# Kernel tuning notes

Hardware: AMD Instinct MI355X
Metric: run time of the kernel (lower is better)

Reference implementation:

```python
import math
import jax, jax.numpy as jnp
import numpy as np

B, T, C = 2, 2048, 4096
H = 32
D = C // H  # head_dim = 128


def compute_freq(dim, max_len, theta=10000):
    freq = 1.0 / theta ** (jnp.arange(0, dim, 2, dtype=jnp.float32) / dim)
    t = jnp.arange(max_len, dtype=jnp.float32)
    m = jnp.einsum('i,j->ij', t, freq)          # [L, dim/2]
    m = jnp.concatenate([m, m], axis=-1)         # [L, dim]
    return jnp.cos(m), jnp.sin(m)


def rotate_half(x):
    # Faithful to source: depth = full last dim, so x1 is the whole tensor
    # and x2 is empty -> rotate_half(x) == x (a quirk of the original code).
    depth = x.shape[-1]
    x1 = x[..., :depth]
    x2 = x[..., depth:]
    return jnp.concatenate([-x2, x1], axis=-1)


def setup_inputs() -> dict:
    key = jax.random.key(0)
    kx, kq, kk, kv, ko = jax.random.split(key, 5)
    std = 0.02
    input_ids = jax.random.normal(kx, (B, T, C), dtype=jnp.float32)
    Wq = jax.random.normal(kq, (C, C), dtype=jnp.float32) * std
    Wk = jax.random.normal(kk, (C, C), dtype=jnp.float32) * std
    Wv = jax.random.normal(kv, (C, C), dtype=jnp.float32) * std
    Wo = jax.random.normal(ko, (C, C), dtype=jnp.float32) * std
    # Additive causal mask, as typically passed to this module.
    causal = jnp.tril(jnp.ones((T, T), dtype=bool))
    attention_mask = jnp.where(causal, 0.0, -1e9).astype(jnp.float32)[None, None]
    return {"input_ids": input_ids, "Wq": Wq, "Wk": Wk, "Wv": Wv,
            "Wo": Wo, "attention_mask": attention_mask}


def reference(input_ids, Wq, Wk, Wv, Wo, attention_mask):
    b, t, c = input_ids.shape
    # QKV projections (no bias), reshape to [b, h, t, d]
    q = (input_ids @ Wq).reshape(b, t, H, D).swapaxes(1, 2)
    k = (input_ids @ Wk).reshape(b, t, H, D).swapaxes(1, 2)
    v = (input_ids @ Wv).reshape(b, t, H, D).swapaxes(1, 2)
    # Inline RoPE (faithful, including the source's rotate_half behavior)
    cos, sin = compute_freq(D, t)                # [t, D]
    q = q * cos + rotate_half(q) * sin
    k = k * cos + rotate_half(k) * sin
    # Naive full attention
    attn = jnp.einsum('bhqd,bhkd->bhqk', q, k) / math.sqrt(D)
    attn = attn + attention_mask
    attn = jax.nn.softmax(attn, axis=-1)
    out = jnp.einsum('bhqk,bhkd->bhqd', attn, v)
    out = out.swapaxes(1, 2).reshape(b, t, c)
    return out @ Wo
```

## Files before the change

kernel.cpp:

```cpp
#include <hip/hip_runtime.h>
#include <hip/hip_bf16.h>

#define B_ 2
#define T_ 2048
#define C_ 4096
#define H_ 32
#define D_ 128

typedef __bf16 bf16x8 __attribute__((ext_vector_type(8)));
typedef float f32x4 __attribute__((ext_vector_type(4)));

__device__ __forceinline__ void gload_lds16(const void* g, void* l) {
  __builtin_amdgcn_global_load_lds(
      (const __attribute__((address_space(1))) void*)g,
      (__attribute__((address_space(3))) void*)l, 16, 0, 0);
}

__device__ __forceinline__ ushort f2bf(float f) {
  union { float f; uint u; } x; x.f = f;
  uint r = x.u + 0x7FFFu + ((x.u >> 16) & 1u);
  return (ushort)(r >> 16);
}

__global__ __launch_bounds__(256) void cvt_f32_bf16(
    const float* __restrict__ in, ushort* __restrict__ out)
{
  long i = ((long)blockIdx.x * 256 + threadIdx.x) * 8;
  float4 a = *(const float4*)&in[i];
  float4 b = *(const float4*)&in[i + 4];
  union { ushort u[8]; uint4 v; } g;
  g.u[0] = f2bf(a.x); g.u[1] = f2bf(a.y); g.u[2] = f2bf(a.z); g.u[3] = f2bf(a.w);
  g.u[4] = f2bf(b.x); g.u[5] = f2bf(b.y); g.u[6] = f2bf(b.z); g.u[7] = f2bf(b.w);
  *(uint4*)&out[i] = g.v;
}

__global__ __launch_bounds__(256) void transpose_f32_bf16(
    const float* __restrict__ in, ushort* __restrict__ out, int ldi, int ldo)
{
  __shared__ __align__(16) ushort tile[64][72];
  const float* ip = in + (long)blockIdx.y * 64 * ldi + (long)blockIdx.x * 64;
  ushort* op = out + (long)blockIdx.x * 64 * ldo + (long)blockIdx.y * 64;
  const int t = threadIdx.x;
  const int row = t >> 2, c0 = (t & 3) * 16;
#pragma unroll
  for (int v = 0; v < 4; ++v) {
    float4 f = *(const float4*)&ip[(long)row * ldi + c0 + v * 4];
    ushort4 w;
    w.x = f2bf(f.x); w.y = f2bf(f.y); w.z = f2bf(f.z); w.w = f2bf(f.w);
    *(ushort4*)&tile[row][c0 + v * 4] = w;
  }
  __syncthreads();
#pragma unroll
  for (int i = 0; i < 2; ++i) {
    int t2 = i * 256 + t;
    int orow = t2 >> 3, ch = t2 & 7;
    union { ushort u[8]; uint4 v; } g;
#pragma unroll
    for (int e = 0; e < 8; ++e) g.u[e] = tile[ch * 8 + e][orow];
    *(uint4*)&op[(long)orow * ldo + ch * 8] = g.v;
  }
}

__global__ __launch_bounds__(256) void transpose_bf16(
    const ushort* __restrict__ in, ushort* __restrict__ out,
    int ldi, int ldo, long zi1, long zi2, long zo1, long zo2)
{
  __shared__ __align__(16) ushort tile[64][72];
  const int z = blockIdx.z;
  const long z1 = z & 31, z2 = z >> 5;
  const ushort* ip = in + z1 * zi1 + z2 * zi2 +
                     (long)blockIdx.y * 64 * ldi + (long)blockIdx.x * 64;
  ushort* op = out + z1 * zo1 + z2 * zo2 +
               (long)blockIdx.x * 64 * ldo + (long)blockIdx.y * 64;
  const int t = threadIdx.x;
#pragma unroll
  for (int i = 0; i < 2; ++i) {
    int t2 = i * 256 + t;
    int row = t2 >> 3, ch = t2 & 7;
    *(uint4*)&tile[row][ch * 8] = *(const uint4*)&ip[(long)row * ldi + ch * 8];
  }
  __syncthreads();
#pragma unroll
  for (int i = 0; i < 2; ++i) {
    int t2 = i * 256 + t;
    int orow = t2 >> 3, ch = t2 & 7;
    union { ushort u[8]; uint4 v; } g;
#pragma unroll
    for (int e = 0; e < 8; ++e) g.u[e] = tile[ch * 8 + e][orow];
    *(uint4*)&op[(long)orow * ldo + ch * 8] = g.v;
  }
}

#define STAGE_A(h, tt) do {                                                    \
    __hip_bfloat16* dst_ = AS + ((((tt) & 1) * 2 + (h)) * 8192) + w * 512;     \
    const __hip_bfloat16* src_ = Asrc + (size_t)((h) * 128) * K + (size_t)(tt) * 64; \
    gload_lds16(src_, dst_);                                                   \
    gload_lds16(src_ + (size_t)64 * K, dst_ + 4096);                           \
  } while (0)

#define STAGE_B(h, tt) do {                                                    \
    __hip_bfloat16* dst_ = BS + ((((tt) & 1) * 2 + (h)) * 8192) + w * 512;     \
    const __hip_bfloat16* src_ = Bsrc + (size_t)((h) * 128) * K + (size_t)(tt) * 64; \
    gload_lds16(src_, dst_);                                                   \
    gload_lds16(src_ + (size_t)64 * K, dst_ + 4096);                           \
  } while (0)

#define MFMA16(pM, pN, AF, BF)                                                 \
  _Pragma("unroll")                                                            \
  for (int mf = 0; mf < 4; ++mf)                                               \
    _Pragma("unroll")                                                          \
    for (int nf = 0; nf < 2; ++nf)                                             \
      _Pragma("unroll")                                                        \
      for (int ks = 0; ks < 2; ++ks)                                           \
        acc[pM][pN][mf][nf] = __builtin_amdgcn_mfma_f32_16x16x32_bf16(         \
            AF[mf][ks], BF[nf][ks], acc[pM][pN][mf][nf], 0, 0, 0);

template <typename OutT>
__global__ __launch_bounds__(512, 2) void gemm256(
    const __hip_bfloat16* __restrict__ A,
    const __hip_bfloat16* __restrict__ Bt,
    OutT* __restrict__ C,
    int M, int N, int K, int rope_mode)
{
  extern __shared__ __hip_bfloat16 smem[];
  __hip_bfloat16* AS = smem;
  __hip_bfloat16* BS = smem + 32768;

  const int tid = threadIdx.x, lane = tid & 63, w = tid >> 6;
  const int wm = w >> 2, wn = w & 3;
  const int fr = lane & 15, quad = lane >> 4;

  const int bid = blockIdx.x;
  const int s = (bid & 7) * 32 + (bid >> 3);
  const int m0 = (s >> 4) * 256, n0 = (s & 15) * 256;

  const int srow = tid >> 3;
  const int schunk = ((tid & 7) ^ (srow & 7)) * 8;
  const __hip_bfloat16* Asrc = A + (size_t)(m0 + srow) * K + schunk;
  const __hip_bfloat16* Bsrc = Bt + (size_t)(n0 + srow) * K + schunk;

  f32x4 acc[2][2][4][2] = {};

  STAGE_A(0, 0); STAGE_B(0, 0); STAGE_A(1, 0); STAGE_B(1, 0);
  STAGE_A(0, 1); STAGE_B(0, 1); STAGE_A(1, 1); STAGE_B(1, 1);
  asm volatile("s_waitcnt vmcnt(8)" ::: "memory");
  asm volatile("s_barrier" ::: "memory");

  const int NT = K >> 6;
  for (int t = 0; t < NT; ++t) {
    const __hip_bfloat16* As0 = AS + (t & 1) * 16384;
    const __hip_bfloat16* Bs0 = BS + (t & 1) * 16384;
    bf16x8 af[4][2], b0[2][2], b1[2][2];

#pragma unroll
    for (int mf = 0; mf < 4; ++mf) {
      const int row = wm * 64 + mf * 16 + fr;
#pragma unroll
      for (int ks = 0; ks < 2; ++ks)
        af[mf][ks] = *(const bf16x8*)
            &As0[row * 64 + (((ks * 4 + quad) ^ (fr & 7)) << 3)];
    }
#pragma unroll
    for (int nf = 0; nf < 2; ++nf) {
      const int row = wn * 32 + nf * 16 + fr;
#pragma unroll
      for (int ks = 0; ks < 2; ++ks)
        b0[nf][ks] = *(const bf16x8*)
            &Bs0[row * 64 + (((ks * 4 + quad) ^ (fr & 7)) << 3)];
    }
    asm volatile("s_barrier" ::: "memory");
    asm volatile("s_waitcnt lgkmcnt(0)" ::: "memory");
    __builtin_amdgcn_sched_barrier(0);
    __builtin_amdgcn_s_setprio(1);
    MFMA16(0, 0, af, b0)
    __builtin_amdgcn_s_setprio(0);
    __builtin_amdgcn_sched_barrier(0);
    asm volatile("s_barrier" ::: "memory");

#pragma unroll
    for (int nf = 0; nf < 2; ++nf) {
      const int row = wn * 32 + nf * 16 + fr;
#pragma unroll
      for (int ks = 0; ks < 2; ++ks)
        b1[nf][ks] = *(const bf16x8*)
            &Bs0[8192 + row * 64 + (((ks * 4 + quad) ^ (fr & 7)) << 3)];
    }
    if (t + 2 < NT) { STAGE_B(0, t + 2); STAGE_A(0, t + 2); }
    asm volatile("s_barrier" ::: "memory");
    asm volatile("s_waitcnt lgkmcnt(0)" ::: "memory");
    __builtin_amdgcn_sched_barrier(0);
    __builtin_amdgcn_s_setprio(1);
    MFMA16(0, 1, af, b1)
    __builtin_amdgcn_s_setprio(0);
    __builtin_amdgcn_sched_barrier(0);
    asm volatile("s_barrier" ::: "memory");

#pragma unroll
    for (int mf = 0; mf < 4; ++mf) {
      const int row = wm * 64 + mf * 16 + fr;
#pragma unroll
      for (int ks = 0; ks < 2; ++ks)
        af[mf][ks] = *(const bf16x8*)
            &As0[8192 + row * 64 + (((ks * 4 + quad) ^ (fr & 7)) << 3)];
    }
    if (t + 2 < NT) STAGE_B(1, t + 2);
    asm volatile("s_barrier" ::: "memory");
    asm volatile("s_waitcnt lgkmcnt(0)" ::: "memory");
    __builtin_amdgcn_sched_barrier(0);
    __builtin_amdgcn_s_setprio(1);
    MFMA16(1, 1, af, b1)
    __builtin_amdgcn_s_setprio(0);
    __builtin_amdgcn_sched_barrier(0);
    asm volatile("s_barrier" ::: "memory");

    if (t + 2 < NT) STAGE_A(1, t + 2);
    if (t < NT - 2) asm volatile("s_waitcnt vmcnt(8)" ::: "memory");
    else            asm volatile("s_waitcnt vmcnt(0)" ::: "memory");
    asm volatile("s_barrier" ::: "memory");
    __builtin_amdgcn_sched_barrier(0);
    __builtin_amdgcn_s_setprio(1);
    MFMA16(1, 0, af, b0)
    __builtin_amdgcn_s_setprio(0);
    __builtin_amdgcn_sched_barrier(0);
    asm volatile("s_barrier" ::: "memory");
  }

  const float gscale = (rope_mode == 1) ? 0.08838834764831845f : 1.0f;
  float freqv[2] = {0.f, 0.f};
  if (rope_mode) {
#pragma unroll
    for (int nf = 0; nf < 2; ++nf)
      freqv[nf] = exp2f((float)((wn & 1) * 32 + nf * 16 + fr) *
                        -0.20762050593046012f);
  }
#pragma unroll
  for (int pM = 0; pM < 2; ++pM)
#pragma unroll
    for (int mf = 0; mf < 4; ++mf)
#pragma unroll
      for (int r = 0; r < 4; ++r) {
        const int grow = m0 + pM * 128 + wm * 64 + mf * 16 + quad * 4 + r;
        float fct[2] = {1.f, 1.f};
        if (rope_mode) {
          const int tt = grow & (T_ - 1);
#pragma unroll
          for (int nf = 0; nf < 2; ++nf) {
            float sn, cs;
            sincosf((float)tt * freqv[nf], &sn, &cs);
            fct[nf] = (cs + sn) * gscale;
          }
        }
#pragma unroll
        for (int pN = 0; pN < 2; ++pN)
#pragma unroll
          for (int nf = 0; nf < 2; ++nf) {
            const int col = n0 + pN * 128 + wn * 32 + nf * 16 + fr;
            float v = acc[pM][pN][mf][nf][r] * fct[nf];
            if constexpr (sizeof(OutT) == 4)
              C[(size_t)grow * N + col] = v;
            else
              C[(size_t)grow * N + col] = __float2bfloat16(v);
          }
      }
}

__global__ __launch_bounds__(256, 3) void flash_attn(
    const __hip_bfloat16* __restrict__ Q,
    const __hip_bfloat16* __restrict__ K,
    const __hip_bfloat16* __restrict__ Vt,
    __hip_bfloat16* __restrict__ O)
{
  __shared__ __align__(16) __hip_bfloat16 Ks[128 * 128];
  __shared__ __align__(16) __hip_bfloat16 Ps[4][32 * 64];
  const int tid = threadIdx.x, lane = tid & 63, wid = tid >> 6;
  const int bx = blockIdx.x, bh = blockIdx.y;
  const int b = bh >> 5, h = bh & 31;
  const int fr = lane & 15, fq = (lane >> 4) * 8;
  const int quad = lane >> 4;
  const __hip_bfloat16* Kbase = K + (size_t)(b * T_) * C_ + h * D_;
  const __hip_bfloat16* Vbase = Vt + (size_t)bh * D_ * T_;

  const int strow = wid * 32 + quad;

  for (int pass = 0; pass < 2; ++pass) {
    const int qt = pass ? (15 - bx) : bx;
    const int q0 = qt * 128;
    const __hip_bfloat16* Qbase = Q + (size_t)(b * T_ + q0) * C_ + h * D_;

#pragma unroll
    for (int j = 0; j < 8; ++j) {
      const int swz = quad + (j & 1) * 4;
      gload_lds16(Qbase + (size_t)(strow + j * 4) * C_ + ((fr ^ swz) * 8),
                  &Ks[(wid * 8 + j) * 512]);
    }
    __syncthreads();
    bf16x8 qf[2][4];
#pragma unroll
    for (int mi = 0; mi < 2; ++mi)
#pragma unroll
      for (int ks = 0; ks < 4; ++ks)
        qf[mi][ks] = *(const bf16x8*)&Ks[(wid * 32 + mi * 16 + fr) * 128 +
                                         (((ks * 4 + quad) ^ (fr & 7)) << 3)];
    __syncthreads();

    float m_i[2][4], l_i[2][4];
#pragma unroll
    for (int mi = 0; mi < 2; ++mi)
#pragma unroll
      for (int r = 0; r < 4; ++r) { m_i[mi][r] = -1e30f; l_i[mi][r] = 0.f; }
    f32x4 oa[2][8] = {};

    for (int kt = 0; kt <= qt; ++kt) {
#pragma unroll
      for (int j = 0; j < 8; ++j) {
        const int swz = quad + (j & 1) * 4;
        gload_lds16(
            Kbase + (size_t)(kt * 128 + strow + j * 4) * C_ + ((fr ^ swz) * 8),
            &Ks[(wid * 8 + j) * 512]);
      }
      __syncthreads();

      f32x4 s[2][8] = {};
#pragma unroll
      for (int ks = 0; ks < 4; ++ks) {
        bf16x8 kf[8];
#pragma unroll
        for (int ni = 0; ni < 8; ++ni)
          kf[ni] = *(const bf16x8*)&Ks[(ni * 16 + fr) * 128 +
                                       (((ks * 4 + quad) ^ (fr & 7)) << 3)];
        __builtin_amdgcn_s_setprio(1);
#pragma unroll
        for (int mi = 0; mi < 2; ++mi)
#pragma unroll
          for (int ni = 0; ni < 8; ++ni)
            s[mi][ni] = __builtin_amdgcn_mfma_f32_16x16x32_bf16(
                qf[mi][ks], kf[ni], s[mi][ni], 0, 0, 0);
        __builtin_amdgcn_s_setprio(0);
      }
      __syncthreads();

#pragma unroll
      for (int j = 0; j < 8; ++j) {
        const int swz = quad + (j & 1) * 4;
        gload_lds16(
            Vbase + (size_t)(strow + j * 4) * T_ + kt * 128 + ((fr ^ swz) * 8),
            &Ks[(wid * 8 + j) * 512]);
      }

      if (kt == qt) {
#pragma unroll
        for (int mi = 0; mi < 2; ++mi)
#pragma unroll
          for (int ni = 0; ni < 8; ++ni)
#pragma unroll
            for (int r = 0; r < 4; ++r) {
              int rl = wid * 32 + mi * 16 + quad * 4 + r;
              int cl = ni * 16 + fr;
              if (cl > rl) s[mi][ni][r] = -1e30f;
            }
      }

#pragma unroll
      for (int mi = 0; mi < 2; ++mi)
#pragma unroll
        for (int r = 0; r < 4; ++r) {
          float mx = -1e30f;
#pragma unroll
          for (int ni = 0; ni < 8; ++ni) mx = fmaxf(mx, s[mi][ni][r]);
          mx = fmaxf(mx, __shfl_xor(mx, 1, 16));
          mx = fmaxf(mx, __shfl_xor(mx, 2, 16));
          mx = fmaxf(mx, __shfl_xor(mx, 4, 16));
          mx = fmaxf(mx, __shfl_xor(mx, 8, 16));
          float mnew = fmaxf(m_i[mi][r], mx);
          float alpha = __expf(m_i[mi][r] - mnew);
          float rs = 0.f;
#pragma unroll
          for (int ni = 0; ni < 8; ++ni) {
            float p = __expf(s[mi][ni][r] - mnew);
            s[mi][ni][r] = p;
            rs += p;
          }
          rs += __shfl_xor(rs, 1, 16);
          rs += __shfl_xor(rs, 2, 16);
          rs += __shfl_xor(rs, 4, 16);
          rs += __shfl_xor(rs, 8, 16);
          m_i[mi][r] = mnew;
          l_i[mi][r] = l_i[mi][r] * alpha + rs;
#pragma unroll
          for (int ni = 0; ni < 8; ++ni) oa[mi][ni][r] *= alpha;
        }

#pragma unroll
      for (int hh = 0; hh < 2; ++hh) {
#pragma unroll
        for (int mi = 0; mi < 2; ++mi)
#pragma unroll
          for (int l = 0; l < 4; ++l) {
            const int sw = (l ^ quad) & 3;
#pragma unroll
            for (int r = 0; r < 4; ++r)
              Ps[wid][(mi * 16 + quad * 4 + r) * 64 + sw * 16 + fr] =
                  __float2bfloat16(s[mi][hh * 4 + l][r]);
          }
        if (hh == 0) __syncthreads();
#pragma unroll
        for (int kl = 0; kl < 2; ++kl) {
          const int ks = hh * 2 + kl;
          bf16x8 pf[2], vf[8];
#pragma unroll
          for (int mi = 0; mi < 2; ++mi) {
            const int rowl = mi * 16 + fr;
            const int sw = ((kl * 2 + (quad >> 1)) ^ ((fr >> 2) & 3)) & 3;
            pf[mi] = *(const bf16x8*)
                &Ps[wid][rowl * 64 + sw * 16 + (quad & 1) * 8];
          }
#pragma unroll
          for (int ni = 0; ni < 8; ++ni)
            vf[ni] = *(const bf16x8*)&Ks[(ni * 16 + fr) * 128 +
                                         (((ks * 4 + quad) ^ (fr & 7)) << 3)];
          __builtin_amdgcn_s_setprio(1);
#pragma unroll
          for (int mi = 0; mi < 2; ++mi)
#pragma unroll
            for (int ni = 0; ni < 8; ++ni)
              oa[mi][ni] = __builtin_amdgcn_mfma_f32_16x16x32_bf16(
                  pf[mi], vf[ni], oa[mi][ni], 0, 0, 0);
          __builtin_amdgcn_s_setprio(0);
        }
      }
      __syncthreads();
    }

#pragma unroll
    for (int mi = 0; mi < 2; ++mi)
#pragma unroll
      for (int r = 0; r < 4; ++r) {
        float inv = 1.f / l_i[mi][r];
        int grow = b * T_ + q0 + wid * 32 + mi * 16 + quad * 4 + r;
#pragma unroll
        for (int ni = 0; ni < 8; ++ni)
          O[(size_t)grow * C_ + h * D_ + ni * 16 + fr] =
              __float2bfloat16(oa[mi][ni][r] * inv);
      }
  }
}

extern "C" void kernel_launch(void* const* d_in, const int* in_sizes, int n_in,
                              void* d_out, int out_size, void* d_ws, size_t ws_size,
                              hipStream_t stream) {
  const float* X  = (const float*)d_in[0];
  const float* Wq = (const float*)d_in[1];
  const float* Wk = (const float*)d_in[2];
  const float* Wv = (const float*)d_in[3];
  const float* Wo = (const float*)d_in[4];
  float* out = (float*)d_out;

  char* ws = (char*)d_ws;
  const size_t SZ = (size_t)4096 * 4096 * 2;
  __hip_bfloat16* Xb  = (__hip_bfloat16*)(ws);
  __hip_bfloat16* Wt  = (__hip_bfloat16*)(ws + SZ);
  __hip_bfloat16* Qb  = (__hip_bfloat16*)(ws + 2 * SZ);
  __hip_bfloat16* Kb  = (__hip_bfloat16*)(ws + 3 * SZ);
  __hip_bfloat16* Vb  = (__hip_bfloat16*)(ws + 4 * SZ);
  __hip_bfloat16* Vtb = Xb;
  __hip_bfloat16* Ob  = Vb;

  const dim3 blk(256);
  const dim3 gT(64, 64, 1);

  hipFuncSetAttribute(reinterpret_cast<const void*>(&gemm256<__hip_bfloat16>),
                      hipFuncAttributeMaxDynamicSharedMemorySize, 131072);
  hipFuncSetAttribute(reinterpret_cast<const void*>(&gemm256<float>),
                      hipFuncAttributeMaxDynamicSharedMemorySize, 131072);

  cvt_f32_bf16<<<8192, blk, 0, stream>>>(X, (ushort*)Xb);

  transpose_f32_bf16<<<gT, blk, 0, stream>>>(Wq, (ushort*)Wt, 4096, 4096);
  gemm256<__hip_bfloat16><<<dim3(256), dim3(512), 131072, stream>>>(
      Xb, Wt, Qb, 4096, 4096, 4096, 1);
  transpose_f32_bf16<<<gT, blk, 0, stream>>>(Wk, (ushort*)Wt, 4096, 4096);
  gemm256<__hip_bfloat16><<<dim3(256), dim3(512), 131072, stream>>>(
      Xb, Wt, Kb, 4096, 4096, 4096, 2);
  transpose_f32_bf16<<<gT, blk, 0, stream>>>(Wv, (ushort*)Wt, 4096, 4096);
  gemm256<__hip_bfloat16><<<dim3(256), dim3(512), 131072, stream>>>(
      Xb, Wt, Vb, 4096, 4096, 4096, 0);

  transpose_bf16<<<dim3(2, 32, 64), blk, 0, stream>>>(
      (const ushort*)Vb, (ushort*)Vtb, 4096, 2048,
       128,  8388608,  262144,  8388608);

  flash_attn<<<dim3(8, 64), blk, 0, stream>>>(Qb, Kb, Vtb, Ob);

  transpose_f32_bf16<<<gT, blk, 0, stream>>>(Wo, (ushort*)Wt, 4096, 4096);
  gemm256<float><<<dim3(256), dim3(512), 131072, stream>>>(
      Ob, Wt, out, 4096, 4096, 4096, 0);
}
```

Before: 1.238 ms.

## Double-buffer K and V tiles in flash attention with prefetch and vmcnt waits

Adds a separate LDS buffer for V so the K tile and the V tile can be in flight together. The next K tile is prefetched while softmax and PV run, and full __syncthreads are replaced with partial vmcnt/lgkmcnt waits plus raw barriers. The goal is to hide global-load latency behind MFMA work. In exchange LDS use roughly doubles and launch bounds drop from 3 to 2 blocks per CU, which reduces occupancy. The hand-written waitcnt counts are fragile if the compiler reorders loads.

Result: faster. 1.061 ms (-14.3%).

```diff
diff --git a/kernel.cpp b/kernel.cpp
--- a/kernel.cpp
+++ b/kernel.cpp
@@ -264,18 +264,19 @@
       }
 }
 
-__global__ __launch_bounds__(256, 3) void flash_attn(
+__global__ __launch_bounds__(256, 2) void flash_attn(
     const __hip_bfloat16* __restrict__ Q,
     const __hip_bfloat16* __restrict__ K,
     const __hip_bfloat16* __restrict__ Vt,
     __hip_bfloat16* __restrict__ O)
 {
   __shared__ __align__(16) __hip_bfloat16 Ks[128 * 128];
+  __shared__ __align__(16) __hip_bfloat16 Vs[128 * 128];
   __shared__ __align__(16) __hip_bfloat16 Ps[4][32 * 64];
   const int tid = threadIdx.x, lane = tid & 63, wid = tid >> 6;
   const int bx = blockIdx.x, bh = blockIdx.y;
   const int b = bh >> 5, h = bh & 31;
-  const int fr = lane & 15, fq = (lane >> 4) * 8;
+  const int fr = lane & 15;
   const int quad = lane >> 4;
   const __hip_bfloat16* Kbase = K + (size_t)(b * T_) * C_ + h * D_;
   const __hip_bfloat16* Vbase = Vt + (size_t)bh * D_ * T_;
@@ -291,17 +292,25 @@
     for (int j = 0; j < 8; ++j) {
       const int swz = quad + (j & 1) * 4;
       gload_lds16(Qbase + (size_t)(strow + j * 4) * C_ + ((fr ^ swz) * 8),
+                  &Vs[(wid * 8 + j) * 512]);
+    }
+#pragma unroll
+    for (int j = 0; j < 8; ++j) {
+      const int swz = quad + (j & 1) * 4;
+      gload_lds16(Kbase + (size_t)(strow + j * 4) * C_ + ((fr ^ swz) * 8),
                   &Ks[(wid * 8 + j) * 512]);
     }
-    __syncthreads();
+    asm volatile("s_waitcnt vmcnt(8)" ::: "memory");
+    asm volatile("s_barrier" ::: "memory");
     bf16x8 qf[2][4];
 #pragma unroll
     for (int mi = 0; mi < 2; ++mi)
 #pragma unroll
       for (int ks = 0; ks < 4; ++ks)
-        qf[mi][ks] = *(const bf16x8*)&Ks[(wid * 32 + mi * 16 + fr) * 128 +
+        qf[mi][ks] = *(const bf16x8*)&Vs[(wid * 32 + mi * 16 + fr) * 128 +
                                          (((ks * 4 + quad) ^ (fr & 7)) << 3)];
-    __syncthreads();
+    asm volatile("s_waitcnt lgkmcnt(0)" ::: "memory");
+    asm volatile("s_barrier" ::: "memory");
 
     float m_i[2][4], l_i[2][4];
 #pragma unroll
@@ -315,10 +324,11 @@
       for (int j = 0; j < 8; ++j) {
         const int swz = quad + (j & 1) * 4;
         gload_lds16(
-            Kbase + (size_t)(kt * 128 + strow + j * 4) * C_ + ((fr ^ swz) * 8),
-            &Ks[(wid * 8 + j) * 512]);
-      }
-      __syncthreads();
+            Vbase + (size_t)(strow + j * 4) * T_ + kt * 128 + ((fr ^ swz) * 8),
+            &Vs[(wid * 8 + j) * 512]);
+      }
+      asm volatile("s_waitcnt vmcnt(8)" ::: "memory");
+      asm volatile("s_barrier" ::: "memory");
 
       f32x4 s[2][8] = {};
 #pragma unroll
@@ -337,14 +347,18 @@
                 qf[mi][ks], kf[ni], s[mi][ni], 0, 0, 0);
         __builtin_amdgcn_s_setprio(0);
       }
-      __syncthreads();
-
-#pragma unroll
-      for (int j = 0; j < 8; ++j) {
-        const int swz = quad + (j & 1) * 4;
-        gload_lds16(
-            Vbase + (size_t)(strow + j * 4) * T_ + kt * 128 + ((fr ^ swz) * 8),
-            &Ks[(wid * 8 + j) * 512]);
+      asm volatile("s_waitcnt lgkmcnt(0)" ::: "memory");
+      asm volatile("s_barrier" ::: "memory");
+
+      if (kt < qt) {
+#pragma unroll
+        for (int j = 0; j < 8; ++j) {
+          const int swz = quad + (j & 1) * 4;
+          gload_lds16(Kbase +
+                          (size_t)((kt + 1) * 128 + strow + j * 4) * C_ +
+                          ((fr ^ swz) * 8),
+                      &Ks[(wid * 8 + j) * 512]);
+        }
       }
 
       if (kt == qt) {
@@ -391,18 +405,33 @@
         }
 
 #pragma unroll
+      for (int mi = 0; mi < 2; ++mi)
+#pragma unroll
+        for (int l = 0; l < 4; ++l) {
+          const int sw = (l ^ quad) & 3;
+#pragma unroll
+          for (int r = 0; r < 4; ++r)
+            Ps[wid][(mi * 16 + quad * 4 + r) * 64 + sw * 16 + fr] =
+                __float2bfloat16(s[mi][l][r]);
+        }
+      if (kt < qt) asm volatile("s_waitcnt vmcnt(8)" ::: "memory");
+      else         asm volatile("s_waitcnt vmcnt(0)" ::: "memory");
+      asm volatile("s_barrier" ::: "memory");
+
+#pragma unroll
       for (int hh = 0; hh < 2; ++hh) {
-#pragma unroll
-        for (int mi = 0; mi < 2; ++mi)
-#pragma unroll
-          for (int l = 0; l < 4; ++l) {
-            const int sw = (l ^ quad) & 3;
-#pragma unroll
-            for (int r = 0; r < 4; ++r)
-              Ps[wid][(mi * 16 + quad * 4 + r) * 64 + sw * 16 + fr] =
-                  __float2bfloat16(s[mi][hh * 4 + l][r]);
-          }
-        if (hh == 0) __syncthreads();
+        if (hh == 1) {
+#pragma unroll
+          for (int mi = 0; mi < 2; ++mi)
+#pragma unroll
+            for (int l = 0; l < 4; ++l) {
+              const int sw = (l ^ quad) & 3;
+#pragma unroll
+              for (int r = 0; r < 4; ++r)
+                Ps[wid][(mi * 16 + quad * 4 + r) * 64 + sw * 16 + fr] =
+                    __float2bfloat16(s[mi][4 + l][r]);
+            }
+        }
 #pragma unroll
         for (int kl = 0; kl < 2; ++kl) {
           const int ks = hh * 2 + kl;
@@ -416,7 +445,7 @@
           }
 #pragma unroll
           for (int ni = 0; ni < 8; ++ni)
-            vf[ni] = *(const bf16x8*)&Ks[(ni * 16 + fr) * 128 +
+            vf[ni] = *(const bf16x8*)&Vs[(ni * 16 + fr) * 128 +
                                          (((ks * 4 + quad) ^ (fr & 7)) << 3)];
           __builtin_amdgcn_s_setprio(1);
 #pragma unroll
@@ -428,7 +457,8 @@
           __builtin_amdgcn_s_setprio(0);
         }
       }
-      __syncthreads();
+      asm volatile("s_waitcnt lgkmcnt(0)" ::: "memory");
+      asm volatile("s_barrier" ::: "memory");
     }
 
 #pragma unroll
```
